# Performance work log

Hardware: AMD Instinct MI355X
Metric: run time of the kernel (lower is better)

The kernel has to match this reference:

```python
import jax, jax.numpy as jnp
import numpy as np

N_ITEM = 80000
N_USER = 20000
D = 128
N_REL = 3
E = 1600000  # edges per relation (~avg degree 16 over N=100000 nodes)


def setup_inputs() -> dict:
    key = jax.random.key(0)
    ks = jax.random.split(key, 10)
    N = N_ITEM + N_USER
    s = 1.0 / np.sqrt(D).astype(np.float32)
    return {
        "h_item": jax.random.normal(ks[0], (N_ITEM, D), jnp.float32),
        "h_user": jax.random.normal(ks[1], (N_USER, D), jnp.float32),
        "W_rel": jax.random.normal(ks[2], (N_REL, D, D), jnp.float32) * s,
        "W_item": jax.random.normal(ks[3], (D, D), jnp.float32) * s,
        "b_item": jax.random.normal(ks[4], (D,), jnp.float32) * s,
        "W_user": jax.random.normal(ks[5], (D, D), jnp.float32) * s,
        "b_user": jax.random.normal(ks[6], (D,), jnp.float32) * s,
        "vals": jax.random.uniform(ks[7], (N_REL, E), jnp.float32),
        "rows": jax.random.randint(ks[8], (N_REL, E), 0, N, jnp.int32),
        "cols": jax.random.randint(ks[9], (N_REL, E), 0, N, jnp.int32),
    }


def reference(h_item, h_user, W_rel, W_item, b_item, W_user, b_user, vals, rows, cols):
    N_i = h_item.shape[0]
    N = N_i + h_user.shape[0]
    h_all = jnp.concatenate([h_item, h_user], axis=0)  # [N, D]
    msg = jnp.zeros_like(h_all)
    # loop over small fixed set of relations (structurally distinct weights)
    for r in range(W_rel.shape[0]):
        hr = h_all @ W_rel[r].T                      # lin_r[r](h_all), bias=False
        # sparse.mm(A_r, hr): gather source rows, scale by edge value, scatter-add to dest
        m = jax.ops.segment_sum(hr[cols[r]] * vals[r][:, None], rows[r], num_segments=N)
        msg = msg + m
    h_item_out = jax.nn.relu((msg[:N_i] + h_item) @ W_item.T + b_item)
    h_user_out = jax.nn.relu((msg[N_i:] + h_user) @ W_user.T + b_user)
    return h_item_out, h_user_out
```

## Files before the change

### kernel.cpp

```cpp
#include <hip/hip_runtime.h>
#include <cstdint>

#define D 128
#define BK 64
#define CAP 1536
#define CHUNK 4096
#define NBK_MAX 1568

typedef short   bf8_t    __attribute__((ext_vector_type(8)));
typedef float   f4_t     __attribute__((ext_vector_type(4)));
typedef unsigned short u8x16_t __attribute__((ext_vector_type(8)));

__device__ __forceinline__ float bf2f(unsigned short u) {
    unsigned v = ((unsigned)u) << 16; float f; __builtin_memcpy(&f, &v, 4); return f;
}
__device__ __forceinline__ unsigned short f2bf(float f) {
    unsigned v; __builtin_memcpy(&v, &f, 4);
    v = v + 0x7FFFu + ((v >> 16) & 1u);
    return (unsigned short)(v >> 16);
}

__global__ __launch_bounds__(256) void convert_kernel(
    const float* __restrict__ h_item, const float* __restrict__ h_user,
    unsigned short* __restrict__ h_bf, int Ni, int N)
{
    int idx = blockIdx.x * 256 + threadIdx.x;
    size_t base = (size_t)idx * 8;
    int row = idx >> 4;
    u8x16_t us = {};
    if (row < N) {
        const float* src = (row < Ni) ? h_item + base
                                      : h_user + (base - (size_t)Ni * D);
        float4 a0 = *reinterpret_cast<const float4*>(src);
        float4 a1 = *reinterpret_cast<const float4*>(src + 4);
        us[0]=f2bf(a0.x); us[1]=f2bf(a0.y); us[2]=f2bf(a0.z); us[3]=f2bf(a0.w);
        us[4]=f2bf(a1.x); us[5]=f2bf(a1.y); us[6]=f2bf(a1.z); us[7]=f2bf(a1.w);
    }
    *reinterpret_cast<u8x16_t*>(h_bf + base) = us;
}

__global__ __launch_bounds__(256) void place_kernel(
    const int* __restrict__ rows, const int* __restrict__ cols,
    const float* __restrict__ vals, int* __restrict__ bcnt,
    uint2* __restrict__ ev, int E, int nbk)
{
    __shared__ int cnt[NBK_MAX];
    __shared__ int base[NBK_MAX];
    const int tid = threadIdx.x;
    const int e0 = blockIdx.x * CHUNK;
    const int ecnt = min(CHUNK, E - e0);

    for (int b = tid; b < nbk; b += 256) cnt[b] = 0;
    __syncthreads();
    for (int i = tid; i < ecnt; i += 256)
        atomicAdd(&cnt[rows[e0 + i] >> 6], 1);
    __syncthreads();
    for (int b = tid; b < nbk; b += 256) {
        int c = cnt[b];
        base[b] = c ? atomicAdd(&bcnt[b * 16], c) : 0;
        cnt[b] = 0;
    }
    __syncthreads();
    for (int i = tid; i < ecnt; i += 256) {
        int r = rows[e0 + i];
        int b = r >> 6;
        int pos = base[b] + atomicAdd(&cnt[b], 1);
        if (pos < CAP)
            ev[(size_t)b * CAP + pos] =
                make_uint2(((unsigned)(r & 63) << 17) | (unsigned)cols[e0 + i],
                           __float_as_uint(vals[e0 + i]));
    }
}

__global__ __launch_bounds__(256) void sort_kernel(
    const int* __restrict__ bcnt, uint2* __restrict__ ev,
    int* __restrict__ rstart, int* __restrict__ rend, int N)
{
    __shared__ uint2 se[CAP];
    __shared__ int hist[BK], cur[BK];
    const int tid = threadIdx.x;
    const int b = blockIdx.x;
    const int cnt = min(bcnt[b * 16], CAP);

    for (int i = tid; i < cnt; i += 256) se[i] = ev[(size_t)b * CAP + i];
    if (tid < BK) hist[tid] = 0;
    __syncthreads();
    for (int i = tid; i < cnt; i += 256)
        atomicAdd(&hist[se[i].x >> 17], 1);
    __syncthreads();
    if (tid < BK) {
        int x = hist[tid], orig = x;
        #pragma unroll
        for (int d = 1; d < 64; d <<= 1) {
            int y = __shfl_up(x, d);
            if (tid >= d) x += y;
        }
        cur[tid] = x - orig;
        int g = b * BK + tid;
        if (g < N) {
            rstart[g] = b * CAP + x - orig;
            rend[g]   = b * CAP + x;
        }
    }
    __syncthreads();
    for (int i = tid; i < cnt; i += 256) {
        uint2 x = se[i];
        int pos = atomicAdd(&cur[x.x >> 17], 1);
        ev[(size_t)b * CAP + pos] = make_uint2(x.x & 0x1FFFFu, x.y);
    }
}

template<int FIRST>
__global__ __launch_bounds__(256) void accum_row(
    const unsigned short* __restrict__ hr, const uint2* __restrict__ ev,
    const int* __restrict__ rstart, const int* __restrict__ rend,
    const unsigned short* __restrict__ h_bf, unsigned short* __restrict__ X,
    int N)
{
    int row = blockIdx.x * 4 + (threadIdx.x >> 6);
    if (row >= N) return;
    const int lane = threadIdx.x & 63;
    int s = rstart[row], t = rend[row];

    float a0, a1;
    if (FIRST) {
        ushort2 hv = *reinterpret_cast<const ushort2*>(h_bf + (size_t)row * D + lane * 2);
        a0 = bf2f(hv.x); a1 = bf2f(hv.y);
    } else {
        if (s == t) return;
        ushort2 xv = *reinterpret_cast<const ushort2*>(X + (size_t)row * D + lane * 2);
        a0 = bf2f(xv.x); a1 = bf2f(xv.y);
    }

    int p = s;
    uint2 e0, e1, e2, e3;
    if (p + 4 <= t) { e0 = ev[p]; e1 = ev[p+1]; e2 = ev[p+2]; e3 = ev[p+3]; }
    while (p + 4 <= t) {
        ushort2 g0 = *reinterpret_cast<const ushort2*>(hr + ((size_t)e0.x << 7) + lane * 2);
        ushort2 g1 = *reinterpret_cast<const ushort2*>(hr + ((size_t)e1.x << 7) + lane * 2);
        ushort2 g2 = *reinterpret_cast<const ushort2*>(hr + ((size_t)e2.x << 7) + lane * 2);
        ushort2 g3 = *reinterpret_cast<const ushort2*>(hr + ((size_t)e3.x << 7) + lane * 2);
        int pn = p + 4;
        uint2 f0 = e0, f1 = e1, f2 = e2, f3 = e3;
        if (pn + 4 <= t) { f0 = ev[pn]; f1 = ev[pn+1]; f2 = ev[pn+2]; f3 = ev[pn+3]; }
        a0 = fmaf(__uint_as_float(e0.y), bf2f(g0.x), a0);
        a1 = fmaf(__uint_as_float(e0.y), bf2f(g0.y), a1);
        a0 = fmaf(__uint_as_float(e1.y), bf2f(g1.x), a0);
        a1 = fmaf(__uint_as_float(e1.y), bf2f(g1.y), a1);
        a0 = fmaf(__uint_as_float(e2.y), bf2f(g2.x), a0);
        a1 = fmaf(__uint_as_float(e2.y), bf2f(g2.y), a1);
        a0 = fmaf(__uint_as_float(e3.y), bf2f(g3.x), a0);
        a1 = fmaf(__uint_as_float(e3.y), bf2f(g3.y), a1);
        e0 = f0; e1 = f1; e2 = f2; e3 = f3;
        p = pn;
    }
    for (; p < t; ++p) {
        uint2 ee = ev[p];
        ushort2 g = *reinterpret_cast<const ushort2*>(hr + ((size_t)ee.x << 7) + lane * 2);
        a0 = fmaf(__uint_as_float(ee.y), bf2f(g.x), a0);
        a1 = fmaf(__uint_as_float(ee.y), bf2f(g.y), a1);
    }
    *reinterpret_cast<ushort2*>(X + (size_t)row * D + lane * 2) =
        make_ushort2(f2bf(a0), f2bf(a1));
}

template<int FINAL>
__global__ __launch_bounds__(256) void gemm128(
    const unsigned short* __restrict__ A, const float* __restrict__ Wf,
    const float* __restrict__ biasp, void* __restrict__ outp, int Mvalid)
{
    __shared__ char LDS[2 * 128 * 272];
    char* As = LDS;
    char* Bs = LDS + 128 * 272;
    const int tid  = threadIdx.x;
    const int lane = tid & 63;
    const int wv   = tid >> 6;
    const int row0 = blockIdx.x * 128;

    #pragma unroll
    for (int i = 0; i < 8; ++i) {
        int idx = i * 256 + tid;
        int r = idx >> 4, u = idx & 15;
        const float* wp = Wf + r * D + u * 8;
        float4 w0 = *reinterpret_cast<const float4*>(wp);
        float4 w1 = *reinterpret_cast<const float4*>(wp + 4);
        u8x16_t us;
        us[0]=f2bf(w0.x); us[1]=f2bf(w0.y); us[2]=f2bf(w0.z); us[3]=f2bf(w0.w);
        us[4]=f2bf(w1.x); us[5]=f2bf(w1.y); us[6]=f2bf(w1.z); us[7]=f2bf(w1.w);
        *reinterpret_cast<u8x16_t*>(&Bs[r * 272 + u * 16]) = us;
    }
    #pragma unroll
    for (int i = 0; i < 8; ++i) {
        int idx = i * 256 + tid;
        int r = idx >> 4, u = idx & 15;
        u8x16_t us = *reinterpret_cast<const u8x16_t*>(
            A + (size_t)(row0 + r) * D + u * 8);
        *reinterpret_cast<u8x16_t*>(&As[r * 272 + u * 16]) = us;
    }
    __syncthreads();

    const int wm = wv >> 1, wn = wv & 1;
    f4_t acc[4][4] = {};

    #pragma unroll
    for (int kk = 0; kk < 4; ++kk) {
        const int ku = kk * 4 + (lane >> 4);
        bf8_t a[4], bfr[4];
        #pragma unroll
        for (int mi = 0; mi < 4; ++mi) {
            int r = wm * 64 + mi * 16 + (lane & 15);
            a[mi] = *reinterpret_cast<const bf8_t*>(&As[r * 272 + ku * 16]);
        }
        #pragma unroll
        for (int nj = 0; nj < 4; ++nj) {
            int r = wn * 64 + nj * 16 + (lane & 15);
            bfr[nj] = *reinterpret_cast<const bf8_t*>(&Bs[r * 272 + ku * 16]);
        }
        #pragma unroll
        for (int mi = 0; mi < 4; ++mi)
            #pragma unroll
            for (int nj = 0; nj < 4; ++nj)
                acc[mi][nj] = __builtin_amdgcn_mfma_f32_16x16x32_bf16(
                    a[mi], bfr[nj], acc[mi][nj], 0, 0, 0);
    }
    __syncthreads();

    if (FINAL == 0) {
        #pragma unroll
        for (int mi = 0; mi < 4; ++mi)
            #pragma unroll
            for (int nj = 0; nj < 4; ++nj)
                #pragma unroll
                for (int q = 0; q < 4; ++q) {
                    int r = wm * 64 + mi * 16 + (lane >> 4) * 4 + q;
                    int c = wn * 64 + nj * 16 + (lane & 15);
                    *reinterpret_cast<unsigned short*>(&As[r * 272 + c * 2]) =
                        f2bf(acc[mi][nj][q]);
                }
        __syncthreads();
        #pragma unroll
        for (int i = 0; i < 8; ++i) {
            int idx = i * 256 + tid;
            int r = idx >> 4, u = idx & 15;
            u8x16_t v = *reinterpret_cast<const u8x16_t*>(&As[r * 272 + u * 16]);
            *reinterpret_cast<u8x16_t*>(
                (unsigned short*)outp + (size_t)(row0 + r) * D + u * 8) = v;
        }
    } else {
        #pragma unroll
        for (int mi = 0; mi < 4; ++mi)
            #pragma unroll
            for (int nj = 0; nj < 4; ++nj)
                #pragma unroll
                for (int q = 0; q < 4; ++q) {
                    int r = wm * 64 + mi * 16 + (lane >> 4) * 4 + q;
                    int c = wn * 64 + nj * 16 + (lane & 15);
                    *reinterpret_cast<float*>(&LDS[r * 544 + c * 4]) = acc[mi][nj][q];
                }
        __syncthreads();
        #pragma unroll
        for (int i = 0; i < 16; ++i) {
            int idx = i * 256 + tid;
            int r = idx >> 5, u = idx & 31;
            int gr = row0 + r;
            if (gr < Mvalid) {
                f4_t v = *reinterpret_cast<const f4_t*>(&LDS[r * 544 + u * 16]);
                float4 bb = *reinterpret_cast<const float4*>(biasp + u * 4);
                v[0] = fmaxf(v[0] + bb.x, 0.f);
                v[1] = fmaxf(v[1] + bb.y, 0.f);
                v[2] = fmaxf(v[2] + bb.z, 0.f);
                v[3] = fmaxf(v[3] + bb.w, 0.f);
                *reinterpret_cast<f4_t*>((float*)outp + (size_t)gr * D + u * 4) = v;
            }
        }
    }
}

extern "C" void kernel_launch(void* const* d_in, const int* in_sizes, int n_in,
                              void* d_out, int out_size, void* d_ws, size_t ws_size,
                              hipStream_t stream)
{
    const float* h_item = (const float*)d_in[0];
    const float* h_user = (const float*)d_in[1];
    const float* W_rel  = (const float*)d_in[2];
    const float* W_item = (const float*)d_in[3];
    const float* b_item = (const float*)d_in[4];
    const float* W_user = (const float*)d_in[5];
    const float* b_user = (const float*)d_in[6];
    const float* vals   = (const float*)d_in[7];
    const int*   rows   = (const int*)d_in[8];
    const int*   cols   = (const int*)d_in[9];

    const int Ni = in_sizes[0] / D;
    const int Nu = in_sizes[1] / D;
    const int N  = Ni + Nu;
    const int NR = in_sizes[2] / (D * D);
    const int E  = in_sizes[7] / NR;
    const int MPAD = ((N + 127) / 128) * 128;
    const int NBKP = MPAD / BK;
    const int nbk  = (N + BK - 1) / BK;

    auto align_up = [](size_t x) { return (x + 255) & ~(size_t)255; };
    char* p = (char*)d_ws;
    unsigned short* h_bf = (unsigned short*)p; p += align_up((size_t)MPAD * D * 2);
    unsigned short* X    = (unsigned short*)p; p += align_up((size_t)MPAD * D * 2);
    unsigned short* hr   = (unsigned short*)p; p += align_up((size_t)MPAD * D * 2);
    uint2* ev            = (uint2*)p;          p += align_up((size_t)NBKP * CAP * 8);
    int*   bcnt3         = (int*)p;            p += align_up((size_t)3 * NBKP * 16 * 4);
    int*   rstart        = (int*)p;            p += align_up((size_t)N * 4);
    int*   rend          = (int*)p;            p += align_up((size_t)N * 4);
    float* out = (float*)d_out;

    hipMemsetAsync(bcnt3, 0, (size_t)3 * NBKP * 16 * sizeof(int), stream);
    convert_kernel<<<MPAD * 16 / 256, 256, 0, stream>>>(h_item, h_user, h_bf, Ni, N);

    const int pblocks = (E + CHUNK - 1) / CHUNK;
    for (int r = 0; r < NR; ++r) {
        int* bcnt = bcnt3 + (size_t)r * NBKP * 16;
        gemm128<0><<<MPAD / 128, 256, 0, stream>>>(
            h_bf, W_rel + (size_t)r * D * D, nullptr, hr, 0);
        place_kernel<<<pblocks, 256, 0, stream>>>(
            rows + (size_t)r * E, cols + (size_t)r * E, vals + (size_t)r * E,
            bcnt, ev, E, nbk);
        sort_kernel<<<nbk, 256, 0, stream>>>(bcnt, ev, rstart, rend, N);
        if (r == 0)
            accum_row<1><<<(N + 3) / 4, 256, 0, stream>>>(
                hr, ev, rstart, rend, h_bf, X, N);
        else
            accum_row<0><<<(N + 3) / 4, 256, 0, stream>>>(
                hr, ev, rstart, rend, h_bf, X, N);
    }

    gemm128<1><<<(Ni + 127) / 128, 256, 0, stream>>>(X, W_item, b_item, out, Ni);
    gemm128<1><<<(MPAD - Ni) / 128, 256, 0, stream>>>(
        X + (size_t)Ni * D, W_user, b_user, out + (size_t)Ni * D, Nu);
}
```

Measured before the change: 513.9 us.

## Batch edge bucketing across relations, fuse input conversion into GEMM, deepen gather unroll

The separate fp32-to-bf16 convert kernel is removed. The relation GEMM now converts h_item/h_user while loading its A tile, and the first accumulation pass reads the fp32 residual directly. When the workspace is large enough, the place and sort kernels run once for all three relations using a 2D grid instead of once per relation, which cuts launches and gives each launch more parallelism. The gather loop is unrolled from 4 to 8 edges for more memory-level parallelism, and the per-bucket capacity drops from 1536 to 1216, which shrinks the sort kernel's LDS and the edge buffer. The cost is a repeated fp32 read and conversion in each of the three GEMMs, and a higher risk that the smaller capacity overflows and silently drops edges.

```diff
diff --git a/kernel.cpp b/kernel.cpp
--- a/kernel.cpp
+++ b/kernel.cpp
@@ -3,7 +3,7 @@
 
 #define D 128
 #define BK 64
-#define CAP 1536
+#define CAP 1216
 #define CHUNK 4096
 #define NBK_MAX 1568
 
@@ -20,32 +20,20 @@
     return (unsigned short)(v >> 16);
 }
 
-__global__ __launch_bounds__(256) void convert_kernel(
-    const float* __restrict__ h_item, const float* __restrict__ h_user,
-    unsigned short* __restrict__ h_bf, int Ni, int N)
-{
-    int idx = blockIdx.x * 256 + threadIdx.x;
-    size_t base = (size_t)idx * 8;
-    int row = idx >> 4;
-    u8x16_t us = {};
-    if (row < N) {
-        const float* src = (row < Ni) ? h_item + base
-                                      : h_user + (base - (size_t)Ni * D);
-        float4 a0 = *reinterpret_cast<const float4*>(src);
-        float4 a1 = *reinterpret_cast<const float4*>(src + 4);
-        us[0]=f2bf(a0.x); us[1]=f2bf(a0.y); us[2]=f2bf(a0.z); us[3]=f2bf(a0.w);
-        us[4]=f2bf(a1.x); us[5]=f2bf(a1.y); us[6]=f2bf(a1.z); us[7]=f2bf(a1.w);
-    }
-    *reinterpret_cast<u8x16_t*>(h_bf + base) = us;
-}
-
 __global__ __launch_bounds__(256) void place_kernel(
     const int* __restrict__ rows, const int* __restrict__ cols,
-    const float* __restrict__ vals, int* __restrict__ bcnt,
-    uint2* __restrict__ ev, int E, int nbk)
+    const float* __restrict__ vals, int* __restrict__ bcnt3,
+    uint2* __restrict__ ev0, int E, int nbk, int relBase, size_t evStride)
 {
     __shared__ int cnt[NBK_MAX];
     __shared__ int base[NBK_MAX];
+    const int rel = relBase + blockIdx.y;
+    const int* rowsR = rows + (size_t)rel * E;
+    const int* colsR = cols + (size_t)rel * E;
+    const float* valsR = vals + (size_t)rel * E;
+    int* bcnt = bcnt3 + (size_t)rel * NBK_MAX * 16;
+    uint2* ev = ev0 + (size_t)rel * evStride;
+
     const int tid = threadIdx.x;
     const int e0 = blockIdx.x * CHUNK;
     const int ecnt = min(CHUNK, E - e0);
@@ -53,7 +41,7 @@
     for (int b = tid; b < nbk; b += 256) cnt[b] = 0;
     __syncthreads();
     for (int i = tid; i < ecnt; i += 256)
-        atomicAdd(&cnt[rows[e0 + i] >> 6], 1);
+        atomicAdd(&cnt[rowsR[e0 + i] >> 6], 1);
     __syncthreads();
     for (int b = tid; b < nbk; b += 256) {
         int c = cnt[b];
@@ -62,25 +50,30 @@
     }
     __syncthreads();
     for (int i = tid; i < ecnt; i += 256) {
-        int r = rows[e0 + i];
+        int r = rowsR[e0 + i];
         int b = r >> 6;
         int pos = base[b] + atomicAdd(&cnt[b], 1);
         if (pos < CAP)
             ev[(size_t)b * CAP + pos] =
-                make_uint2(((unsigned)(r & 63) << 17) | (unsigned)cols[e0 + i],
-                           __float_as_uint(vals[e0 + i]));
+                make_uint2(((unsigned)(r & 63) << 17) | (unsigned)colsR[e0 + i],
+                           __float_as_uint(valsR[e0 + i]));
     }
 }
 
 __global__ __launch_bounds__(256) void sort_kernel(
-    const int* __restrict__ bcnt, uint2* __restrict__ ev,
-    int* __restrict__ rstart, int* __restrict__ rend, int N)
+    const int* __restrict__ bcnt3, uint2* __restrict__ ev0,
+    int* __restrict__ rstart3, int* __restrict__ rend3,
+    int N, int relBase, size_t evStride)
 {
     __shared__ uint2 se[CAP];
     __shared__ int hist[BK], cur[BK];
+    const int rel = relBase + blockIdx.y;
     const int tid = threadIdx.x;
     const int b = blockIdx.x;
-    const int cnt = min(bcnt[b * 16], CAP);
+    const int cnt = min(bcnt3[(size_t)rel * NBK_MAX * 16 + b * 16], CAP);
+    uint2* ev = ev0 + (size_t)rel * evStride;
+    int* rstart = rstart3 + (size_t)rel * N;
+    int* rend   = rend3   + (size_t)rel * N;
 
     for (int i = tid; i < cnt; i += 256) se[i] = ev[(size_t)b * CAP + i];
     if (tid < BK) hist[tid] = 0;
@@ -114,8 +107,8 @@
 __global__ __launch_bounds__(256) void accum_row(
     const unsigned short* __restrict__ hr, const uint2* __restrict__ ev,
     const int* __restrict__ rstart, const int* __restrict__ rend,
-    const unsigned short* __restrict__ h_bf, unsigned short* __restrict__ X,
-    int N)
+    const float* __restrict__ h_item, const float* __restrict__ h_user,
+    unsigned short* __restrict__ X, int N, int Ni)
 {
     int row = blockIdx.x * 4 + (threadIdx.x >> 6);
     if (row >= N) return;
@@ -124,8 +117,10 @@
 
     float a0, a1;
     if (FIRST) {
-        ushort2 hv = *reinterpret_cast<const ushort2*>(h_bf + (size_t)row * D + lane * 2);
-        a0 = bf2f(hv.x); a1 = bf2f(hv.y);
+        const float* hsrc = (row < Ni) ? h_item + (size_t)row * D
+                                       : h_user + (size_t)(row - Ni) * D;
+        float2 hv = *reinterpret_cast<const float2*>(hsrc + lane * 2);
+        a0 = hv.x; a1 = hv.y;
     } else {
         if (s == t) return;
         ushort2 xv = *reinterpret_cast<const ushort2*>(X + (size_t)row * D + lane * 2);
@@ -133,30 +128,39 @@
     }
 
     int p = s;
-    uint2 e0, e1, e2, e3;
-    if (p + 4 <= t) { e0 = ev[p]; e1 = ev[p+1]; e2 = ev[p+2]; e3 = ev[p+3]; }
-    while (p + 4 <= t) {
-        ushort2 g0 = *reinterpret_cast<const ushort2*>(hr + ((size_t)e0.x << 7) + lane * 2);
-        ushort2 g1 = *reinterpret_cast<const ushort2*>(hr + ((size_t)e1.x << 7) + lane * 2);
-        ushort2 g2 = *reinterpret_cast<const ushort2*>(hr + ((size_t)e2.x << 7) + lane * 2);
-        ushort2 g3 = *reinterpret_cast<const ushort2*>(hr + ((size_t)e3.x << 7) + lane * 2);
-        int pn = p + 4;
-        uint2 f0 = e0, f1 = e1, f2 = e2, f3 = e3;
-        if (pn + 4 <= t) { f0 = ev[pn]; f1 = ev[pn+1]; f2 = ev[pn+2]; f3 = ev[pn+3]; }
-        a0 = fmaf(__uint_as_float(e0.y), bf2f(g0.x), a0);
-        a1 = fmaf(__uint_as_float(e0.y), bf2f(g0.y), a1);
-        a0 = fmaf(__uint_as_float(e1.y), bf2f(g1.x), a0);
-        a1 = fmaf(__uint_as_float(e1.y), bf2f(g1.y), a1);
-        a0 = fmaf(__uint_as_float(e2.y), bf2f(g2.x), a0);
-        a1 = fmaf(__uint_as_float(e2.y), bf2f(g2.y), a1);
-        a0 = fmaf(__uint_as_float(e3.y), bf2f(g3.x), a0);
-        a1 = fmaf(__uint_as_float(e3.y), bf2f(g3.y), a1);
-        e0 = f0; e1 = f1; e2 = f2; e3 = f3;
-        p = pn;
+    if (p + 8 <= t) {
+        uint2 e[8];
+        #pragma unroll
+        for (int j = 0; j < 8; ++j) e[j] = ev[p + j];
+        while (true) {
+            ushort2 g[8];
+            #pragma unroll
+            for (int j = 0; j < 8; ++j)
+                g[j] = *reinterpret_cast<const ushort2*>(
+                    hr + ((size_t)e[j].x << 7) + lane * 2);
+            int pn = p + 8;
+            bool more = (pn + 8 <= t);
+            uint2 f[8];
+            if (more) {
+                #pragma unroll
+                for (int j = 0; j < 8; ++j) f[j] = ev[pn + j];
+            }
+            #pragma unroll
+            for (int j = 0; j < 8; ++j) {
+                float v = __uint_as_float(e[j].y);
+                a0 = fmaf(v, bf2f(g[j].x), a0);
+                a1 = fmaf(v, bf2f(g[j].y), a1);
+            }
+            p = pn;
+            if (!more) break;
+            #pragma unroll
+            for (int j = 0; j < 8; ++j) e[j] = f[j];
+        }
     }
     for (; p < t; ++p) {
         uint2 ee = ev[p];
-        ushort2 g = *reinterpret_cast<const ushort2*>(hr + ((size_t)ee.x << 7) + lane * 2);
+        ushort2 g = *reinterpret_cast<const ushort2*>(
+            hr + ((size_t)ee.x << 7) + lane * 2);
         a0 = fmaf(__uint_as_float(ee.y), bf2f(g.x), a0);
         a1 = fmaf(__uint_as_float(ee.y), bf2f(g.y), a1);
     }
@@ -164,10 +168,11 @@
         make_ushort2(f2bf(a0), f2bf(a1));
 }
 
-template<int FINAL>
+template<int AMODE, int FINAL>
 __global__ __launch_bounds__(256) void gemm128(
-    const unsigned short* __restrict__ A, const float* __restrict__ Wf,
-    const float* __restrict__ biasp, void* __restrict__ outp, int Mvalid)
+    const void* __restrict__ Aptr, const void* __restrict__ A2ptr,
+    const float* __restrict__ Wf, const float* __restrict__ biasp,
+    void* __restrict__ outp, int Ni, int Ntot, int Mvalid)
 {
     __shared__ char LDS[2 * 128 * 272];
     char* As = LDS;
@@ -193,8 +198,22 @@
     for (int i = 0; i < 8; ++i) {
         int idx = i * 256 + tid;
         int r = idx >> 4, u = idx & 15;
-        u8x16_t us = *reinterpret_cast<const u8x16_t*>(
-            A + (size_t)(row0 + r) * D + u * 8);
+        int gr = row0 + r;
+        u8x16_t us = {};
+        if (AMODE == 0) {
+            if (gr < Ntot) {
+                const float* hp = (gr < Ni)
+                    ? (const float*)Aptr  + (size_t)gr * D
+                    : (const float*)A2ptr + (size_t)(gr - Ni) * D;
+                float4 a0 = *reinterpret_cast<const float4*>(hp + u * 8);
+                float4 a1 = *reinterpret_cast<const float4*>(hp + u * 8 + 4);
+                us[0]=f2bf(a0.x); us[1]=f2bf(a0.y); us[2]=f2bf(a0.z); us[3]=f2bf(a0.w);
+                us[4]=f2bf(a1.x); us[5]=f2bf(a1.y); us[6]=f2bf(a1.z); us[7]=f2bf(a1.w);
+            }
+        } else {
+            us = *reinterpret_cast<const u8x16_t*>(
+                (const unsigned short*)Aptr + (size_t)gr * D + u * 8);
+        }
         *reinterpret_cast<u8x16_t*>(&As[r * 272 + u * 16]) = us;
     }
     __syncthreads();
@@ -300,38 +319,57 @@
     const int NBKP = MPAD / BK;
     const int nbk  = (N + BK - 1) / BK;
 
-    auto align_up = [](size_t x) { return (x + 255) & ~(size_t)255; };
+    auto au = [](size_t x) { return (x + 255) & ~(size_t)255; };
+    const size_t xB   = au((size_t)MPAD * D * 2);
+    const size_t hrB  = au((size_t)MPAD * D * 2);
+    const size_t bcB  = au((size_t)3 * NBK_MAX * 16 * 4);
+    const size_t rsB  = au((size_t)3 * N * 4);
+    const size_t evB1 = au((size_t)NBKP * CAP * sizeof(uint2));
+
+    const bool merged = ws_size >= xB + hrB + bcB + 2 * rsB + 3 * evB1;
+
     char* p = (char*)d_ws;
-    unsigned short* h_bf = (unsigned short*)p; p += align_up((size_t)MPAD * D * 2);
-    unsigned short* X    = (unsigned short*)p; p += align_up((size_t)MPAD * D * 2);
-    unsigned short* hr   = (unsigned short*)p; p += align_up((size_t)MPAD * D * 2);
-    uint2* ev            = (uint2*)p;          p += align_up((size_t)NBKP * CAP * 8);
-    int*   bcnt3         = (int*)p;            p += align_up((size_t)3 * NBKP * 16 * 4);
-    int*   rstart        = (int*)p;            p += align_up((size_t)N * 4);
-    int*   rend          = (int*)p;            p += align_up((size_t)N * 4);
+    unsigned short* X  = (unsigned short*)p; p += xB;
+    unsigned short* hr = (unsigned short*)p; p += hrB;
+    int* bcnt3   = (int*)p;   p += bcB;
+    int* rstart3 = (int*)p;   p += rsB;
+    int* rend3   = (int*)p;   p += rsB;
+    uint2* ev    = (uint2*)p;
+    const size_t evStride = merged ? (size_t)NBKP * CAP : 0;
     float* out = (float*)d_out;
 
-    hipMemsetAsync(bcnt3, 0, (size_t)3 * NBKP * 16 * sizeof(int), stream);
-    convert_kernel<<<MPAD * 16 / 256, 256, 0, stream>>>(h_item, h_user, h_bf, Ni, N);
-
     const int pblocks = (E + CHUNK - 1) / CHUNK;
+
+    hipMemsetAsync(bcnt3, 0, (size_t)3 * NBK_MAX * 16 * sizeof(int), stream);
+
+    if (merged) {
+        place_kernel<<<dim3(pblocks, 3), 256, 0, stream>>>(
+            rows, cols, vals, bcnt3, ev, E, nbk, 0, evStride);
+        sort_kernel<<<dim3(nbk, 3), 256, 0, stream>>>(
+            bcnt3, ev, rstart3, rend3, N, 0, evStride);
+    }
+
     for (int r = 0; r < NR; ++r) {
-        int* bcnt = bcnt3 + (size_t)r * NBKP * 16;
-        gemm128<0><<<MPAD / 128, 256, 0, stream>>>(
-            h_bf, W_rel + (size_t)r * D * D, nullptr, hr, 0);
-        place_kernel<<<pblocks, 256, 0, stream>>>(
-            rows + (size_t)r * E, cols + (size_t)r * E, vals + (size_t)r * E,
-            bcnt, ev, E, nbk);
-        sort_kernel<<<nbk, 256, 0, stream>>>(bcnt, ev, rstart, rend, N);
+        if (!merged) {
+            place_kernel<<<dim3(pblocks, 1), 256, 0, stream>>>(
+                rows, cols, vals, bcnt3, ev, E, nbk, r, 0);
+            sort_kernel<<<dim3(nbk, 1), 256, 0, stream>>>(
+                bcnt3, ev, rstart3, rend3, N, r, 0);
+        }
+        gemm128<0, 0><<<MPAD / 128, 256, 0, stream>>>(
+            h_item, h_user, W_rel + (size_t)r * D * D, nullptr, hr, Ni, N, 0);
         if (r == 0)
             accum_row<1><<<(N + 3) / 4, 256, 0, stream>>>(
-                hr, ev, rstart, rend, h_bf, X, N);
+                hr, ev + r * evStride, rstart3 + (size_t)r * N,
+                rend3 + (size_t)r * N, h_item, h_user, X, N, Ni);
         else
             accum_row<0><<<(N + 3) / 4, 256, 0, stream>>>(
-                hr, ev, rstart, rend, h_bf, X, N);
-    }
-
-    gemm128<1><<<(Ni + 127) / 128, 256, 0, stream>>>(X, W_item, b_item, out, Ni);
-    gemm128<1><<<(MPAD - Ni) / 128, 256, 0, stream>>>(
-        X + (size_t)Ni * D, W_user, b_user, out + (size_t)Ni * D, Nu);
-}
+                hr, ev + r * evStride, rstart3 + (size_t)r * N,
+                rend3 + (size_t)r * N, h_item, h_user, X, N, Ni);
+    }
+
+    gemm128<1, 1><<<(Ni + 127) / 128, 256, 0, stream>>>(
+        X, nullptr, W_item, b_item, out, 0, 0, Ni);
+    gemm128<1, 1><<<(MPAD - Ni) / 128, 256, 0, stream>>>(
+        X + (size_t)Ni * D, nullptr, W_user, b_user, out + (size_t)Ni * D, 0, 0, Nu);
+}
```

Measured after the change: 542.8 us, median of 4. 1.06x slower.
